# Kernel optimization log

Hardware: AMD Instinct MI355X
Metric: run time of the kernel (lower is better)

The kernel has to match this reference:

```python
import jax, jax.numpy as jnp
import numpy as np

NUM_HEADS = 8
H_SCALE = 1000.0
WIND_THRESHOLD = 5.0


def setup_inputs() -> dict:
    key = jax.random.key(0)
    ks = jax.random.split(key, 8)
    B, N, C = 8, 1024, 256
    H = W = 64  # (H//2)*(W//2) == N
    x = jax.random.normal(ks[0], (B, N, C), dtype=jnp.float32)
    elevation = jax.random.uniform(ks[1], (B, N), dtype=jnp.float32)
    u_wind = jax.random.normal(ks[2], (B, H, W), dtype=jnp.float32)
    v_wind = jax.random.normal(ks[3], (B, H, W), dtype=jnp.float32)
    w_qkv = jax.random.normal(ks[4], (3 * C, C), dtype=jnp.float32) * (C ** -0.5)
    w_proj = jax.random.normal(ks[5], (C, C), dtype=jnp.float32) * (C ** -0.5)
    b_proj = jnp.zeros((C,), dtype=jnp.float32)
    alpha = jnp.float32(1.0)
    beta = jnp.float32(0.3)
    return {"x": x, "elevation": elevation, "u_wind": u_wind, "v_wind": v_wind,
            "w_qkv": w_qkv, "w_proj": w_proj, "b_proj": b_proj,
            "alpha": alpha, "beta": beta}


def _wind_strength(u_wind, v_wind):
    # 2x2 average pool of wind magnitude -> [B, N]
    B, H, W = u_wind.shape
    mag = jnp.sqrt(u_wind ** 2 + v_wind ** 2 + 1e-8)
    mag = mag.reshape(B, H // 2, 2, W // 2, 2).mean(axis=(2, 4))
    return mag.reshape(B, -1)


def _elevation_bias(elevation, u_wind, v_wind, alpha, beta):
    # elev_diff[b,i,j] = elev[b,j] - elev[b,i]
    elev_diff = elevation[:, None, :] - elevation[:, :, None]
    bias = -alpha * jax.nn.relu(elev_diff / H_SCALE)
    ws = _wind_strength(u_wind, v_wind)  # [B, N]
    wind_factor = jax.nn.sigmoid((ws[:, None, :] + ws[:, :, None]) * 0.5 - WIND_THRESHOLD)
    bias = bias * (1.0 - beta * wind_factor)
    return jnp.clip(bias, -10.0, 0.0)  # [B, N, N]


def reference(x, elevation, u_wind, v_wind, w_qkv, w_proj, b_proj, alpha, beta):
    B, N, C = x.shape
    hd = C // NUM_HEADS
    scale = hd ** -0.5
    qkv = (x @ w_qkv.T).reshape(B, N, 3, NUM_HEADS, hd)
    qkv = jnp.transpose(qkv, (2, 0, 3, 1, 4))  # [3, B, H, N, hd]
    q, k, v = qkv[0], qkv[1], qkv[2]
    scores = jnp.einsum('bhnd,bhmd->bhnm', q, k) * scale
    bias = _elevation_bias(elevation, u_wind, v_wind, alpha, beta)
    scores = scores + bias[:, None, :, :]
    attn = jax.nn.softmax(scores, axis=-1)
    out = jnp.einsum('bhnm,bhmd->bhnd', attn, v)
    out = jnp.transpose(out, (0, 2, 1, 3)).reshape(B, N, C)
    return out @ w_proj.T + b_proj
```

## Files before the change

kernel.cpp:

```cpp
#include <hip/hip_runtime.h>
#include <stdint.h>

typedef __attribute__((ext_vector_type(8))) short short8;
typedef __attribute__((ext_vector_type(8))) __bf16 bf16x8;
typedef __attribute__((ext_vector_type(4))) float f32x4;
typedef __attribute__((ext_vector_type(4))) _Float16 f16x4;
typedef __attribute__((ext_vector_type(4))) unsigned short ushort4_t;
typedef __attribute__((ext_vector_type(2))) unsigned int uint2_t;
typedef __attribute__((ext_vector_type(2))) float float2_t;

__device__ __forceinline__ unsigned short f2bf(float f) {
  unsigned int u = __builtin_bit_cast(unsigned int, f);
  u += 0x7fffu + ((u >> 16) & 1u);
  return (unsigned short)(u >> 16);
}

__device__ __forceinline__ f32x4 mfma16(short8 a, short8 b, f32x4 c) {
  return __builtin_amdgcn_mfma_f32_16x16x32_bf16(
      __builtin_bit_cast(bf16x8, a), __builtin_bit_cast(bf16x8, b), c, 0, 0, 0);
}

__device__ __forceinline__ short8 ld8(const unsigned short* p) {
  return *reinterpret_cast<const short8*>(p);
}

__global__ __launch_bounds__(256) void k_prep(const float* __restrict__ wqkv,
                                              const float* __restrict__ wproj,
                                              const float* __restrict__ u,
                                              const float* __restrict__ v,
                                              unsigned short* __restrict__ wqkv_bf,
                                              unsigned short* __restrict__ wproj_bf,
                                              float* __restrict__ ws) {
  int gx = blockIdx.x, t = threadIdx.x;
  if (gx < 768) {
    int i = gx * 256 + t;
    wqkv_bf[i] = f2bf(wqkv[i]);
  } else if (gx < 1024) {
    int i = (gx - 768) * 256 + t;
    wproj_bf[i] = f2bf(wproj[i]);
  } else {
    int i = (gx - 1024) * 256 + t;
    int b = i >> 10, n = i & 1023;
    int ph = n >> 5, pw = n & 31;
    const float* ub = u + b * 4096;
    const float* vb = v + b * 4096;
    float s = 0.f;
#pragma unroll
    for (int dy = 0; dy < 2; ++dy)
#pragma unroll
      for (int dx = 0; dx < 2; ++dx) {
        int idx = (2 * ph + dy) * 64 + (2 * pw + dx);
        float uu = ub[idx], vv = vb[idx];
        s += sqrtf(uu * uu + vv * vv + 1e-8f);
      }
    ws[i] = s * 0.25f;
  }
}

__global__ __launch_bounds__(256, 4) void k_qkv(const float* __restrict__ x,
                                                const unsigned short* __restrict__ wq_bf,
                                                unsigned short* __restrict__ qb,
                                                unsigned short* __restrict__ kb,
                                                unsigned short* __restrict__ vT) {
  __shared__ unsigned short xs[64][264];
  const int tid = threadIdx.x;
  const int w = tid >> 6, lane = tid & 63;
  const int c = lane & 15, g = lane >> 4;
  const int m0 = blockIdx.y * 64;
  const int n0 = blockIdx.x * 192;
#pragma unroll
  for (int i = 0; i < 16; ++i) {
    int idx = i * 1024 + tid * 4;
    int row = idx >> 8, col = idx & 255;
    f32x4 vv = *reinterpret_cast<const f32x4*>(x + (size_t)(m0 + row) * 256 + col);
    ushort4_t hh;
#pragma unroll
    for (int j = 0; j < 4; ++j) hh[j] = f2bf(vv[j]);
    *reinterpret_cast<ushort4_t*>(&xs[row][col]) = hh;
  }
  __syncthreads();
  f32x4 acc[12] = {};
#pragma unroll
  for (int k0 = 0; k0 < 256; k0 += 32) {
    short8 af = ld8(&xs[w * 16 + c][k0 + g * 8]);
#pragma unroll
    for (int nb = 0; nb < 12; ++nb) {
      short8 bf = ld8(wq_bf + (size_t)(n0 + nb * 16 + c) * 256 + k0 + g * 8);
      acc[nb] = mfma16(af, bf, acc[nb]);
    }
  }
#pragma unroll
  for (int nb = 0; nb < 12; ++nb) {
    int col = n0 + nb * 16 + c;
    int s = col >> 8, rem = col & 255;
    int h = rem >> 5, d = rem & 31;
    int nrow0 = m0 + w * 16 + g * 4;
    int b = nrow0 >> 10, nn = nrow0 & 1023;
    size_t bh = (size_t)(b * 8 + h);
    if (s == 2) {
      ushort4_t pk;
#pragma unroll
      for (int r = 0; r < 4; ++r) pk[r] = f2bf(acc[nb][r]);
      *reinterpret_cast<ushort4_t*>(vT + (bh * 32 + d) * 1024 + nn) = pk;
    } else {
      unsigned short* dst = (s == 0) ? qb : kb;
      float scale = (s == 0) ? 0.17677669529663687f : 1.0f;
#pragma unroll
      for (int r = 0; r < 4; ++r)
        dst[(bh * 1024 + nn + r) * 32 + d] = f2bf(acc[nb][r] * scale);
    }
  }
}

__global__ __launch_bounds__(256, 4) void k_attn(const unsigned short* __restrict__ qb,
                                                 const unsigned short* __restrict__ kb,
                                                 const unsigned short* __restrict__ vT,
                                                 const float* __restrict__ elev,
                                                 const float* __restrict__ wsd,
                                                 const float* __restrict__ alphap,
                                                 const float* __restrict__ betap,
                                                 float* __restrict__ o_part,
                                                 float* __restrict__ ml_part) {
  __shared__ _Float16 bias_lds[2][32][72];
  __shared__ unsigned short p_lds[4][32][72];
  const int tid = threadIdx.x;
  const int w = tid >> 6, lane = tid & 63;
  const int c = lane & 15, g = lane >> 4;
  const int q0 = blockIdx.x * 32, b = blockIdx.y;
  const int hg = blockIdx.z & 1, sp = blockIdx.z >> 1;
  const int h = hg * 4 + w;
  const size_t bh = (size_t)(b * 8 + h);
  const int kvbase = sp * 512;
  const float alpha = alphap[0], beta = betap[0];

  const int sqr = tid >> 3, skv = (tid & 7) * 8;
  const float* eb = elev + b * 1024;
  const float* wb = wsd + b * 1024;
  const float ei = eb[q0 + sqr], wi = wb[q0 + sqr];

  auto stage_bias = [&](int buf, int kv0) {
    f32x4 ej0 = *reinterpret_cast<const f32x4*>(eb + kv0 + skv);
    f32x4 ej1 = *reinterpret_cast<const f32x4*>(eb + kv0 + skv + 4);
    f32x4 wj0 = *reinterpret_cast<const f32x4*>(wb + kv0 + skv);
    f32x4 wj1 = *reinterpret_cast<const f32x4*>(wb + kv0 + skv + 4);
    f16x4 h0, h1;
#pragma unroll
    for (int j = 0; j < 4; ++j) {
      float dd = fmaxf((ej0[j] - ei) * 1e-3f, 0.f);
      float sig = 1.0f / (1.0f + __expf(5.0f - (wi + wj0[j]) * 0.5f));
      h0[j] = (_Float16)fminf(fmaxf(-alpha * dd * (1.0f - beta * sig), -10.0f), 0.0f);
      float dd1 = fmaxf((ej1[j] - ei) * 1e-3f, 0.f);
      float sig1 = 1.0f / (1.0f + __expf(5.0f - (wi + wj1[j]) * 0.5f));
      h1[j] = (_Float16)fminf(fmaxf(-alpha * dd1 * (1.0f - beta * sig1), -10.0f), 0.0f);
    }
    *reinterpret_cast<f16x4*>(&bias_lds[buf][sqr][skv]) = h0;
    *reinterpret_cast<f16x4*>(&bias_lds[buf][sqr][skv + 4]) = h1;
  };

  stage_bias(0, kvbase);

  short8 qf[2];
#pragma unroll
  for (int qs = 0; qs < 2; ++qs)
    qf[qs] = ld8(qb + (bh * 1024 + q0 + qs * 16 + c) * 32 + g * 8);

  f32x4 oacc[2][2] = {};
  float mold[2] = {-1e30f, -1e30f};
  float lrow[2] = {0.f, 0.f};
  __syncthreads();

  for (int t8 = 0; t8 < 8; ++t8) {
    const int buf = t8 & 1;
    const int kv0 = kvbase + t8 * 64;

    short8 kf[4];
#pragma unroll
    for (int t = 0; t < 4; ++t)
      kf[t] = ld8(kb + (bh * 1024 + kv0 + t * 16 + c) * 32 + g * 8);

#pragma unroll
    for (int qs = 0; qs < 2; ++qs) {
      f32x4 z = {};
      f32x4 s[4];
#pragma unroll
      for (int t = 0; t < 4; ++t) s[t] = mfma16(kf[t], qf[qs], z);
      float p[4][4];
      float m16 = -1e30f;
#pragma unroll
      for (int t = 0; t < 4; ++t) {
        f16x4 bv = *reinterpret_cast<const f16x4*>(&bias_lds[buf][qs * 16 + c][t * 16 + 4 * g]);
#pragma unroll
        for (int r = 0; r < 4; ++r) {
          float sv = s[t][r] + (float)bv[r];
          p[t][r] = sv;
          m16 = fmaxf(m16, sv);
        }
      }
      m16 = fmaxf(m16, __shfl_xor(m16, 16));
      m16 = fmaxf(m16, __shfl_xor(m16, 32));
      float mn = fmaxf(mold[qs], m16);
      float corr = __expf(mold[qs] - mn);
      mold[qs] = mn;
      float ps = 0.f;
#pragma unroll
      for (int t = 0; t < 4; ++t)
#pragma unroll
        for (int r = 0; r < 4; ++r) {
          float e = __expf(p[t][r] - mn);
          p[t][r] = e;
          ps += e;
        }
      ps += __shfl_xor(ps, 16);
      ps += __shfl_xor(ps, 32);
      lrow[qs] = lrow[qs] * corr + ps;
#pragma unroll
      for (int hs = 0; hs < 2; ++hs) oacc[qs][hs] *= corr;
#pragma unroll
      for (int t = 0; t < 4; ++t) {
        uint2_t pk;
        pk[0] = (unsigned)f2bf(p[t][0]) | ((unsigned)f2bf(p[t][1]) << 16);
        pk[1] = (unsigned)f2bf(p[t][2]) | ((unsigned)f2bf(p[t][3]) << 16);
        *reinterpret_cast<uint2_t*>(&p_lds[w][qs * 16 + c][t * 16 + 4 * g]) = pk;
      }
    }

#pragma unroll
    for (int t2 = 0; t2 < 2; ++t2) {
      short8 pf[2];
#pragma unroll
      for (int qs = 0; qs < 2; ++qs)
        pf[qs] = ld8(&p_lds[w][qs * 16 + c][t2 * 32 + g * 8]);
#pragma unroll
      for (int hs = 0; hs < 2; ++hs) {
        short8 vf = ld8(vT + (bh * 32 + hs * 16 + c) * 1024 + kv0 + t2 * 32 + g * 8);
#pragma unroll
        for (int qs = 0; qs < 2; ++qs)
          oacc[qs][hs] = mfma16(vf, pf[qs], oacc[qs][hs]);
      }
    }

    if (t8 < 7) stage_bias(buf ^ 1, kv0 + 64);
    __syncthreads();
  }

#pragma unroll
  for (int qs = 0; qs < 2; ++qs) {
    size_t qrow = ((size_t)sp * 64 + bh) * 1024 + q0 + qs * 16 + c;
#pragma unroll
    for (int hs = 0; hs < 2; ++hs)
      *reinterpret_cast<f32x4*>(o_part + qrow * 32 + hs * 16 + 4 * g) = oacc[qs][hs];
    if (g == 0) {
      float2_t ml = {mold[qs], lrow[qs]};
      *reinterpret_cast<float2_t*>(ml_part + qrow * 2) = ml;
    }
  }
}

__global__ __launch_bounds__(256, 2) void k_proj(const float* __restrict__ o_part,
                                                 const float* __restrict__ ml_part,
                                                 const unsigned short* __restrict__ wp_bf,
                                                 const float* __restrict__ bproj,
                                                 float* __restrict__ out) {
  __shared__ unsigned short xs[32][264];
  const int tid = threadIdx.x;
  const int w = tid >> 6, lane = tid & 63;
  const int c = lane & 15, g = lane >> 4;
  const int wm = w & 1, wn = w >> 1;
  const int m0 = blockIdx.x * 32;
  const int b = m0 >> 10, q0 = m0 & 1023;

  const int qq = tid >> 3, d0 = (tid & 7) * 4;
#pragma unroll
  for (int h = 0; h < 8; ++h) {
    size_t r0 = ((size_t)(b * 8 + h) * 1024 + q0 + qq);
    size_t r1 = r0 + (size_t)64 * 1024;
    f32x4 o0 = *reinterpret_cast<const f32x4*>(o_part + r0 * 32 + d0);
    f32x4 o1 = *reinterpret_cast<const f32x4*>(o_part + r1 * 32 + d0);
    float2_t ml0 = *reinterpret_cast<const float2_t*>(ml_part + r0 * 2);
    float2_t ml1 = *reinterpret_cast<const float2_t*>(ml_part + r1 * 2);
    float mm = fmaxf(ml0[0], ml1[0]);
    float a0 = __expf(ml0[0] - mm), a1 = __expf(ml1[0] - mm);
    float inv = 1.0f / (a0 * ml0[1] + a1 * ml1[1]);
    ushort4_t hh;
#pragma unroll
    for (int j = 0; j < 4; ++j) hh[j] = f2bf((o0[j] * a0 + o1[j] * a1) * inv);
    *reinterpret_cast<ushort4_t*>(&xs[qq][h * 32 + d0]) = hh;
  }
  __syncthreads();

  f32x4 acc[8] = {};
#pragma unroll
  for (int k0 = 0; k0 < 256; k0 += 32) {
    short8 af = ld8(&xs[wm * 16 + c][k0 + g * 8]);
#pragma unroll
    for (int nb = 0; nb < 8; ++nb) {
      short8 bf = ld8(wp_bf + (size_t)(wn * 128 + nb * 16 + c) * 256 + k0 + g * 8);
      acc[nb] = mfma16(af, bf, acc[nb]);
    }
  }
#pragma unroll
  for (int nb = 0; nb < 8; ++nb) {
    int col = wn * 128 + nb * 16 + c;
    float bv = bproj[col];
#pragma unroll
    for (int r = 0; r < 4; ++r) {
      int row = m0 + wm * 16 + g * 4 + r;
      out[(size_t)row * 256 + col] = acc[nb][r] + bv;
    }
  }
}

extern "C" void kernel_launch(void* const* d_in, const int* in_sizes, int n_in,
                              void* d_out, int out_size, void* d_ws, size_t ws_size,
                              hipStream_t stream) {
  const float* x = (const float*)d_in[0];
  const float* elev = (const float*)d_in[1];
  const float* uw = (const float*)d_in[2];
  const float* vw = (const float*)d_in[3];
  const float* wqkv = (const float*)d_in[4];
  const float* wproj = (const float*)d_in[5];
  const float* bproj = (const float*)d_in[6];
  const float* alpha = (const float*)d_in[7];
  const float* beta = (const float*)d_in[8];
  float* out = (float*)d_out;

  char* p = (char*)d_ws;
  auto alloc = [&](size_t bytes) {
    char* r = p;
    p += (bytes + 255) & ~(size_t)255;
    return r;
  };
  float* ws_wind = (float*)alloc(8192 * 4);
  unsigned short* wqkv_bf = (unsigned short*)alloc((size_t)768 * 256 * 2);
  unsigned short* wproj_bf = (unsigned short*)alloc((size_t)256 * 256 * 2);
  unsigned short* qb = (unsigned short*)alloc((size_t)2097152 * 2);
  unsigned short* kb = (unsigned short*)alloc((size_t)2097152 * 2);
  unsigned short* vT = (unsigned short*)alloc((size_t)2097152 * 2);
  float* o_part = (float*)alloc((size_t)2 * 2097152 * 4);
  float* ml_part = (float*)alloc((size_t)2 * 65536 * 2 * 4);

  k_prep<<<dim3(1056), dim3(256), 0, stream>>>(wqkv, wproj, uw, vw, wqkv_bf, wproj_bf, ws_wind);
  k_qkv<<<dim3(4, 128), dim3(256), 0, stream>>>(x, wqkv_bf, qb, kb, vT);
  k_attn<<<dim3(32, 8, 4), dim3(256), 0, stream>>>(qb, kb, vT, elev, ws_wind, alpha, beta, o_part, ml_part);
  k_proj<<<dim3(256), dim3(256), 0, stream>>>(o_part, ml_part, wproj_bf, bproj, out);
}
```

Before: 162.8 us.

## Fold softmax scale into weights, use exp2 domain, inject bias via MFMA accumulator

Folds the attention scale and log2(e) into the Q weights during prep, and pre-scales elevation and wind strength so the bias and softmax run in the exp2 domain with hardware exp2/rcp. The bias is kept in fp32 LDS and passed as the MFMA accumulator input, which removes a separate add pass. Rescaling of the running max is skipped when the new max is within a threshold of the old one, and hardware bf16 packing replaces the manual rounding. Each k_qkv block now does two column tiles to halve x staging work. The bias is no longer double-buffered, so an extra barrier is added per KV step, and the lazy max rescale is a numerical trade-off.

```diff
diff --git a/kernel.cpp b/kernel.cpp
--- a/kernel.cpp
+++ b/kernel.cpp
@@ -3,11 +3,12 @@
 
 typedef __attribute__((ext_vector_type(8))) short short8;
 typedef __attribute__((ext_vector_type(8))) __bf16 bf16x8;
+typedef __attribute__((ext_vector_type(2))) __bf16 bf16x2;
 typedef __attribute__((ext_vector_type(4))) float f32x4;
-typedef __attribute__((ext_vector_type(4))) _Float16 f16x4;
-typedef __attribute__((ext_vector_type(4))) unsigned short ushort4_t;
 typedef __attribute__((ext_vector_type(2))) unsigned int uint2_t;
 typedef __attribute__((ext_vector_type(2))) float float2_t;
+
+#define LOG2E 1.44269504f
 
 __device__ __forceinline__ unsigned short f2bf(float f) {
   unsigned int u = __builtin_bit_cast(unsigned int, f);
@@ -15,6 +16,13 @@
   return (unsigned short)(u >> 16);
 }
 
+__device__ __forceinline__ unsigned int pk2(float a, float b) {
+  bf16x2 t;
+  t[0] = (__bf16)a;
+  t[1] = (__bf16)b;
+  return __builtin_bit_cast(unsigned int, t);
+}
+
 __device__ __forceinline__ f32x4 mfma16(short8 a, short8 b, f32x4 c) {
   return __builtin_amdgcn_mfma_f32_16x16x32_bf16(
       __builtin_bit_cast(bf16x8, a), __builtin_bit_cast(bf16x8, b), c, 0, 0, 0);
@@ -28,13 +36,17 @@
                                               const float* __restrict__ wproj,
                                               const float* __restrict__ u,
                                               const float* __restrict__ v,
+                                              const float* __restrict__ elev,
+                                              const float* __restrict__ alphap,
                                               unsigned short* __restrict__ wqkv_bf,
                                               unsigned short* __restrict__ wproj_bf,
-                                              float* __restrict__ ws) {
+                                              float* __restrict__ esc,
+                                              float* __restrict__ wsc) {
   int gx = blockIdx.x, t = threadIdx.x;
   if (gx < 768) {
     int i = gx * 256 + t;
-    wqkv_bf[i] = f2bf(wqkv[i]);
+    float s = (i < 256 * 256) ? (0.17677669529663687f * LOG2E) : 1.0f;
+    wqkv_bf[i] = f2bf(wqkv[i] * s);
   } else if (gx < 1024) {
     int i = (gx - 768) * 256 + t;
     wproj_bf[i] = f2bf(wproj[i]);
@@ -53,7 +65,8 @@
         float uu = ub[idx], vv = vb[idx];
         s += sqrtf(uu * uu + vv * vv + 1e-8f);
       }
-    ws[i] = s * 0.25f;
+    wsc[i] = s * (0.25f * 0.5f * LOG2E);
+    esc[i] = elev[i] * (alphap[0] * 1e-3f * LOG2E);
   }
 }
 
@@ -67,47 +80,47 @@
   const int w = tid >> 6, lane = tid & 63;
   const int c = lane & 15, g = lane >> 4;
   const int m0 = blockIdx.y * 64;
-  const int n0 = blockIdx.x * 192;
 #pragma unroll
   for (int i = 0; i < 16; ++i) {
     int idx = i * 1024 + tid * 4;
     int row = idx >> 8, col = idx & 255;
     f32x4 vv = *reinterpret_cast<const f32x4*>(x + (size_t)(m0 + row) * 256 + col);
-    ushort4_t hh;
-#pragma unroll
-    for (int j = 0; j < 4; ++j) hh[j] = f2bf(vv[j]);
-    *reinterpret_cast<ushort4_t*>(&xs[row][col]) = hh;
+    uint2_t hh = {pk2(vv[0], vv[1]), pk2(vv[2], vv[3])};
+    *reinterpret_cast<uint2_t*>(&xs[row][col]) = hh;
   }
   __syncthreads();
-  f32x4 acc[12] = {};
-#pragma unroll
-  for (int k0 = 0; k0 < 256; k0 += 32) {
-    short8 af = ld8(&xs[w * 16 + c][k0 + g * 8]);
+  for (int nt = 0; nt < 2; ++nt) {
+    const int n0 = blockIdx.x * 384 + nt * 192;
+    f32x4 acc[12] = {};
+#pragma unroll
+    for (int k0 = 0; k0 < 256; k0 += 32) {
+      short8 af = ld8(&xs[w * 16 + c][k0 + g * 8]);
+#pragma unroll
+      for (int nb = 0; nb < 12; ++nb) {
+        short8 bf = ld8(wq_bf + (size_t)(n0 + nb * 16 + c) * 256 + k0 + g * 8);
+        acc[nb] = mfma16(af, bf, acc[nb]);
+      }
+    }
 #pragma unroll
     for (int nb = 0; nb < 12; ++nb) {
-      short8 bf = ld8(wq_bf + (size_t)(n0 + nb * 16 + c) * 256 + k0 + g * 8);
-      acc[nb] = mfma16(af, bf, acc[nb]);
-    }
-  }
-#pragma unroll
-  for (int nb = 0; nb < 12; ++nb) {
-    int col = n0 + nb * 16 + c;
-    int s = col >> 8, rem = col & 255;
-    int h = rem >> 5, d = rem & 31;
-    int nrow0 = m0 + w * 16 + g * 4;
-    int b = nrow0 >> 10, nn = nrow0 & 1023;
-    size_t bh = (size_t)(b * 8 + h);
-    if (s == 2) {
-      ushort4_t pk;
-#pragma unroll
-      for (int r = 0; r < 4; ++r) pk[r] = f2bf(acc[nb][r]);
-      *reinterpret_cast<ushort4_t*>(vT + (bh * 32 + d) * 1024 + nn) = pk;
-    } else {
-      unsigned short* dst = (s == 0) ? qb : kb;
-      float scale = (s == 0) ? 0.17677669529663687f : 1.0f;
-#pragma unroll
-      for (int r = 0; r < 4; ++r)
-        dst[(bh * 1024 + nn + r) * 32 + d] = f2bf(acc[nb][r] * scale);
+      int col = n0 + nb * 16 + c;
+      int s = col >> 8, rem = col & 255;
+      int h = rem >> 5, d = rem & 31;
+      int nrow0 = m0 + w * 16 + g * 4;
+      int b = nrow0 >> 10, nn = nrow0 & 1023;
+      size_t bh = (size_t)(b * 8 + h);
+      if (s == 2) {
+        uint2_t pk = {pk2(acc[nb][0], acc[nb][1]), pk2(acc[nb][2], acc[nb][3])};
+        *reinterpret_cast<uint2_t*>(vT + (bh * 32 + d) * 1024 + nn) = pk;
+      } else {
+        unsigned short* dst = (s == 0) ? qb : kb;
+#pragma unroll
+        for (int r = 0; r < 4; ++r) {
+          bf16x2 one;
+          one[0] = (__bf16)acc[nb][r];
+          dst[(bh * 1024 + nn + r) * 32 + d] = __builtin_bit_cast(unsigned short, one[0]);
+        }
+      }
     }
   }
 }
@@ -115,13 +128,12 @@
 __global__ __launch_bounds__(256, 4) void k_attn(const unsigned short* __restrict__ qb,
                                                  const unsigned short* __restrict__ kb,
                                                  const unsigned short* __restrict__ vT,
-                                                 const float* __restrict__ elev,
-                                                 const float* __restrict__ wsd,
-                                                 const float* __restrict__ alphap,
+                                                 const float* __restrict__ esc,
+                                                 const float* __restrict__ wsc,
                                                  const float* __restrict__ betap,
                                                  float* __restrict__ o_part,
                                                  float* __restrict__ ml_part) {
-  __shared__ _Float16 bias_lds[2][32][72];
+  __shared__ float bias_lds[32][72];
   __shared__ unsigned short p_lds[4][32][72];
   const int tid = threadIdx.x;
   const int w = tid >> 6, lane = tid & 63;
@@ -131,33 +143,37 @@
   const int h = hg * 4 + w;
   const size_t bh = (size_t)(b * 8 + h);
   const int kvbase = sp * 512;
-  const float alpha = alphap[0], beta = betap[0];
+  const float beta = betap[0];
 
   const int sqr = tid >> 3, skv = (tid & 7) * 8;
-  const float* eb = elev + b * 1024;
-  const float* wb = wsd + b * 1024;
-  const float ei = eb[q0 + sqr], wi = wb[q0 + sqr];
-
-  auto stage_bias = [&](int buf, int kv0) {
-    f32x4 ej0 = *reinterpret_cast<const f32x4*>(eb + kv0 + skv);
-    f32x4 ej1 = *reinterpret_cast<const f32x4*>(eb + kv0 + skv + 4);
-    f32x4 wj0 = *reinterpret_cast<const f32x4*>(wb + kv0 + skv);
-    f32x4 wj1 = *reinterpret_cast<const f32x4*>(wb + kv0 + skv + 4);
-    f16x4 h0, h1;
+  const float* ebs = esc + b * 1024;
+  const float* wbs = wsc + b * 1024;
+  const float eisc = ebs[q0 + sqr];
+  const float Kw = 7.2134752f - wbs[q0 + sqr];
+
+  auto bias_elem = [&](float ej, float wj) -> float {
+    float d = fmaxf(ej - eisc, 0.f);
+    float e2 = __builtin_amdgcn_exp2f(Kw - wj);
+    float sig = __builtin_amdgcn_rcpf(1.0f + e2);
+    float bb = d * beta * sig - d;
+    return fminf(fmaxf(bb, -14.4269504f), 0.f);
+  };
+  auto stage_bias = [&](int kv0) {
+    f32x4 ej0 = *reinterpret_cast<const f32x4*>(ebs + kv0 + skv);
+    f32x4 ej1 = *reinterpret_cast<const f32x4*>(ebs + kv0 + skv + 4);
+    f32x4 wj0 = *reinterpret_cast<const f32x4*>(wbs + kv0 + skv);
+    f32x4 wj1 = *reinterpret_cast<const f32x4*>(wbs + kv0 + skv + 4);
+    f32x4 o0, o1;
 #pragma unroll
     for (int j = 0; j < 4; ++j) {
-      float dd = fmaxf((ej0[j] - ei) * 1e-3f, 0.f);
-      float sig = 1.0f / (1.0f + __expf(5.0f - (wi + wj0[j]) * 0.5f));
-      h0[j] = (_Float16)fminf(fmaxf(-alpha * dd * (1.0f - beta * sig), -10.0f), 0.0f);
-      float dd1 = fmaxf((ej1[j] - ei) * 1e-3f, 0.f);
-      float sig1 = 1.0f / (1.0f + __expf(5.0f - (wi + wj1[j]) * 0.5f));
-      h1[j] = (_Float16)fminf(fmaxf(-alpha * dd1 * (1.0f - beta * sig1), -10.0f), 0.0f);
-    }
-    *reinterpret_cast<f16x4*>(&bias_lds[buf][sqr][skv]) = h0;
-    *reinterpret_cast<f16x4*>(&bias_lds[buf][sqr][skv + 4]) = h1;
+      o0[j] = bias_elem(ej0[j], wj0[j]);
+      o1[j] = bias_elem(ej1[j], wj1[j]);
+    }
+    *reinterpret_cast<f32x4*>(&bias_lds[sqr][skv]) = o0;
+    *reinterpret_cast<f32x4*>(&bias_lds[sqr][skv + 4]) = o1;
   };
 
-  stage_bias(0, kvbase);
+  stage_bias(kvbase);
 
   short8 qf[2];
 #pragma unroll
@@ -170,7 +186,6 @@
   __syncthreads();
 
   for (int t8 = 0; t8 < 8; ++t8) {
-    const int buf = t8 & 1;
     const int kv0 = kvbase + t8 * 64;
 
     short8 kf[4];
@@ -180,49 +195,48 @@
 
 #pragma unroll
     for (int qs = 0; qs < 2; ++qs) {
-      f32x4 z = {};
       f32x4 s[4];
 #pragma unroll
-      for (int t = 0; t < 4; ++t) s[t] = mfma16(kf[t], qf[qs], z);
-      float p[4][4];
-      float m16 = -1e30f;
-#pragma unroll
       for (int t = 0; t < 4; ++t) {
-        f16x4 bv = *reinterpret_cast<const f16x4*>(&bias_lds[buf][qs * 16 + c][t * 16 + 4 * g]);
-#pragma unroll
-        for (int r = 0; r < 4; ++r) {
-          float sv = s[t][r] + (float)bv[r];
-          p[t][r] = sv;
-          m16 = fmaxf(m16, sv);
-        }
-      }
+        f32x4 bc = *reinterpret_cast<const f32x4*>(&bias_lds[qs * 16 + c][t * 16 + 4 * g]);
+        s[t] = mfma16(kf[t], qf[qs], bc);
+      }
+      float m16 = fmaxf(fmaxf(fmaxf(s[0][0], s[0][1]), fmaxf(s[0][2], s[0][3])),
+                        fmaxf(fmaxf(s[1][0], s[1][1]), fmaxf(s[1][2], s[1][3])));
+      m16 = fmaxf(m16, fmaxf(fmaxf(fmaxf(s[2][0], s[2][1]), fmaxf(s[2][2], s[2][3])),
+                             fmaxf(fmaxf(s[3][0], s[3][1]), fmaxf(s[3][2], s[3][3]))));
       m16 = fmaxf(m16, __shfl_xor(m16, 16));
       m16 = fmaxf(m16, __shfl_xor(m16, 32));
-      float mn = fmaxf(mold[qs], m16);
-      float corr = __expf(mold[qs] - mn);
-      mold[qs] = mn;
+      if (!__all(m16 <= mold[qs] + 11.0f)) {
+        float mn = fmaxf(mold[qs], m16);
+        float corr = __builtin_amdgcn_exp2f(mold[qs] - mn);
+        mold[qs] = mn;
+        lrow[qs] *= corr;
+        oacc[qs][0] *= corr;
+        oacc[qs][1] *= corr;
+      }
+      float p[4][4];
       float ps = 0.f;
 #pragma unroll
       for (int t = 0; t < 4; ++t)
 #pragma unroll
         for (int r = 0; r < 4; ++r) {
-          float e = __expf(p[t][r] - mn);
+          float e = __builtin_amdgcn_exp2f(s[t][r] - mold[qs]);
           p[t][r] = e;
           ps += e;
         }
       ps += __shfl_xor(ps, 16);
       ps += __shfl_xor(ps, 32);
-      lrow[qs] = lrow[qs] * corr + ps;
-#pragma unroll
-      for (int hs = 0; hs < 2; ++hs) oacc[qs][hs] *= corr;
+      lrow[qs] += ps;
 #pragma unroll
       for (int t = 0; t < 4; ++t) {
-        uint2_t pk;
-        pk[0] = (unsigned)f2bf(p[t][0]) | ((unsigned)f2bf(p[t][1]) << 16);
-        pk[1] = (unsigned)f2bf(p[t][2]) | ((unsigned)f2bf(p[t][3]) << 16);
-        *reinterpret_cast<uint2_t*>(&p_lds[w][qs * 16 + c][t * 16 + 4 * g]) = pk;
-      }
-    }
+        uint2_t pkw = {pk2(p[t][0], p[t][1]), pk2(p[t][2], p[t][3])};
+        *reinterpret_cast<uint2_t*>(&p_lds[w][qs * 16 + c][t * 16 + 4 * g]) = pkw;
+      }
+    }
+
+    __syncthreads();
+    if (t8 < 7) stage_bias(kv0 + 64);
 
 #pragma unroll
     for (int t2 = 0; t2 < 2; ++t2) {
@@ -239,7 +253,6 @@
       }
     }
 
-    if (t8 < 7) stage_bias(buf ^ 1, kv0 + 64);
     __syncthreads();
   }
 
@@ -279,12 +292,14 @@
     float2_t ml0 = *reinterpret_cast<const float2_t*>(ml_part + r0 * 2);
     float2_t ml1 = *reinterpret_cast<const float2_t*>(ml_part + r1 * 2);
     float mm = fmaxf(ml0[0], ml1[0]);
-    float a0 = __expf(ml0[0] - mm), a1 = __expf(ml1[0] - mm);
+    float a0 = __builtin_amdgcn_exp2f(ml0[0] - mm);
+    float a1 = __builtin_amdgcn_exp2f(ml1[0] - mm);
     float inv = 1.0f / (a0 * ml0[1] + a1 * ml1[1]);
-    ushort4_t hh;
-#pragma unroll
-    for (int j = 0; j < 4; ++j) hh[j] = f2bf((o0[j] * a0 + o1[j] * a1) * inv);
-    *reinterpret_cast<ushort4_t*>(&xs[qq][h * 32 + d0]) = hh;
+    f32x4 r;
+#pragma unroll
+    for (int j = 0; j < 4; ++j) r[j] = (o0[j] * a0 + o1[j] * a1) * inv;
+    uint2_t hh = {pk2(r[0], r[1]), pk2(r[2], r[3])};
+    *reinterpret_cast<uint2_t*>(&xs[qq][h * 32 + d0]) = hh;
   }
   __syncthreads();
 
@@ -330,7 +345,8 @@
     p += (bytes + 255) & ~(size_t)255;
     return r;
   };
-  float* ws_wind = (float*)alloc(8192 * 4);
+  float* esc = (float*)alloc(8192 * 4);
+  float* wsc = (float*)alloc(8192 * 4);
   unsigned short* wqkv_bf = (unsigned short*)alloc((size_t)768 * 256 * 2);
   unsigned short* wproj_bf = (unsigned short*)alloc((size_t)256 * 256 * 2);
   unsigned short* qb = (unsigned short*)alloc((size_t)2097152 * 2);
@@ -339,8 +355,9 @@
   float* o_part = (float*)alloc((size_t)2 * 2097152 * 4);
   float* ml_part = (float*)alloc((size_t)2 * 65536 * 2 * 4);
 
-  k_prep<<<dim3(1056), dim3(256), 0, stream>>>(wqkv, wproj, uw, vw, wqkv_bf, wproj_bf, ws_wind);
-  k_qkv<<<dim3(4, 128), dim3(256), 0, stream>>>(x, wqkv_bf, qb, kb, vT);
-  k_attn<<<dim3(32, 8, 4), dim3(256), 0, stream>>>(qb, kb, vT, elev, ws_wind, alpha, beta, o_part, ml_part);
+  k_prep<<<dim3(1056), dim3(256), 0, stream>>>(wqkv, wproj, uw, vw, elev, alpha,
+                                               wqkv_bf, wproj_bf, esc, wsc);
+  k_qkv<<<dim3(2, 128), dim3(256), 0, stream>>>(x, wqkv_bf, qb, kb, vT);
+  k_attn<<<dim3(32, 8, 4), dim3(256), 0, stream>>>(qb, kb, vT, esc, wsc, beta, o_part, ml_part);
   k_proj<<<dim3(256), dim3(256), 0, stream>>>(o_part, ml_part, wproj_bf, bproj, out);
 }
```

Measured after the change: 163.6 us. About the same (+0.5%).
